# Performance work log

Hardware: AMD Instinct MI355X
Metric: run time of the kernel (lower is better)

## Reference

```python
import jax, jax.numpy as jnp
import numpy as np

NUM_NODES, NUM_RELS = 100000, 32
VOCAB = NUM_NODES + NUM_RELS
EMB, HID, LAYERS, CW = 128, 768, 4, 3
NHEAD, HDIM = HID // 64, 64
B, S = 4, 1024
T = S - 4 * CW  # rows where the full banded submask fits
EPS = 1e-5


def setup_inputs() -> dict:
    key = jax.random.key(0)
    ks = jax.random.split(key, 24)
    f32 = jnp.float32
    d = {}
    d["seq"] = jax.random.randint(ks[0], (B, S), 0, VOCAB)
    d["neg_ids"] = jax.random.randint(ks[1], (T, B), 0, VOCAB)
    # embedding + LayerNorm
    d["emb_table"] = jax.random.normal(ks[2], (VOCAB, EMB), f32)
    d["emb_ln_g"] = jnp.ones((EMB,), f32)
    d["emb_ln_b"] = jnp.zeros((EMB,), f32)
    # proj: Linear(EMB->HID) + GELU
    d["proj_w"] = jax.random.normal(ks[3], (HID, EMB), f32) * 0.02
    d["proj_b"] = jnp.zeros((HID,), f32)
    # transformer encoder layers (torch post-norm layout)
    d["wqkv"] = jax.random.normal(ks[4], (LAYERS, 3 * HID, HID), f32) * 0.02
    d["bqkv"] = jnp.zeros((LAYERS, 3 * HID), f32)
    d["wo"] = jax.random.normal(ks[5], (LAYERS, HID, HID), f32) * 0.02
    d["bo"] = jnp.zeros((LAYERS, HID), f32)
    d["ln1_g"] = jnp.ones((LAYERS, HID), f32)
    d["ln1_b"] = jnp.zeros((LAYERS, HID), f32)
    d["w1"] = jax.random.normal(ks[6], (LAYERS, 4 * HID, HID), f32) * 0.02
    d["b1"] = jnp.zeros((LAYERS, 4 * HID), f32)
    d["w2"] = jax.random.normal(ks[7], (LAYERS, HID, 4 * HID), f32) * 0.02
    d["b2"] = jnp.zeros((LAYERS, HID), f32)
    d["ln2_g"] = jnp.ones((LAYERS, HID), f32)
    d["ln2_b"] = jnp.zeros((LAYERS, HID), f32)
    # out: Linear(HID->EMB) + LayerNorm
    d["out_w"] = jax.random.normal(ks[8], (EMB, HID), f32) * 0.02
    d["out_b"] = jnp.zeros((EMB,), f32)
    d["out_ln_g"] = jnp.ones((EMB,), f32)
    d["out_ln_b"] = jnp.zeros((EMB,), f32)
    return d


def _ln(x, g, b):
    m = x.mean(-1, keepdims=True)
    v = x.var(-1, keepdims=True)
    return (x - m) * jax.lax.rsqrt(v + EPS) * g + b


def _pos_encoding(s, h):
    pos = jnp.arange(s, dtype=jnp.float32)[:, None]
    div = jnp.exp(jnp.arange(0, h, 2, dtype=jnp.float32) * (-jnp.log(10000.0) / h))
    ang = pos * div  # (S, H/2)
    pe = jnp.zeros((s, h), jnp.float32)
    pe = pe.at[:, 0::2].set(jnp.sin(ang)).at[:, 1::2].set(jnp.cos(ang))
    return pe[:, None, :]  # (S,1,H)


def _band_mask(s):
    i = jnp.arange(s)[:, None]
    j = jnp.arange(s)[None, :]
    gap = j - i
    allowed = (gap >= 0) & (gap <= 4 * CW) & (gap != 2 * CW)
    return jnp.where(allowed, 0.0, -jnp.inf).astype(jnp.float32)


def reference(seq, neg_ids, emb_table, emb_ln_g, emb_ln_b, proj_w, proj_b,
              wqkv, bqkv, wo, bo, ln1_g, ln1_b, w1, b1, w2, b2, ln2_g, ln2_b,
              out_w, out_b, out_ln_g, out_ln_b):
    seq_t = seq.T  # (S,B)
    s, b = seq_t.shape
    z = _ln(emb_table[seq_t], emb_ln_g, emb_ln_b)                 # (S,B,EMB)
    tokens = jax.nn.gelu(jnp.einsum('sbe,he->sbh', z, proj_w) + proj_b,
                         approximate=False)                        # (S,B,HID)
    tokens = tokens + _pos_encoding(s, HID)
    mask = _band_mask(s)                                           # (S,S)
    scale = 1.0 / jnp.sqrt(jnp.float32(HDIM))
    x = tokens
    for l in range(LAYERS):
        qkv = jnp.einsum('sbh,gh->sbg', x, wqkv[l]) + bqkv[l]      # (S,B,3H)
        q, k, v = [t.reshape(s, b, NHEAD, HDIM)
                   for t in jnp.split(qkv, 3, axis=-1)]
        scores = jnp.einsum('sbhd,tbhd->bhst', q, k) * scale + mask
        a = jax.nn.softmax(scores, axis=-1)                        # (B,H,S,S)
        attn = jnp.einsum('bhst,tbhd->sbhd', a, v).reshape(s, b, HID)
        attn = jnp.einsum('sbh,gh->sbg', attn, wo[l]) + bo[l]
        x = _ln(x + attn, ln1_g[l], ln1_b[l])
        ff = jax.nn.gelu(jnp.einsum('sbh,fh->sbf', x, w1[l]) + b1[l],
                         approximate=False)
        ff = jnp.einsum('sbf,hf->sbh', ff, w2[l]) + b2[l]
        x = _ln(x + ff, ln2_g[l], ln2_b[l])
    z_out = _ln(jnp.einsum('sbh,eh->sbe', x, out_w) + out_b,
                out_ln_g, out_ln_b)                                # (S,B,EMB)
    targets = jnp.arange(T) + CW + 1                               # (T,)
    z_hat = z_out[targets]                                         # (T,B,EMB)
    z_pos = z[targets]
    pos = jnp.sum(z_pos * z_hat, axis=-1).reshape(-1)              # (T*B,)
    z_neg = _ln(emb_table[neg_ids], emb_ln_g, emb_ln_b)            # (T,B,EMB)
    neg = jnp.sum(z_neg * z_hat, axis=-1).reshape(-1)              # (T*B,)
    # BCEWithLogitsLoss: labels 1 for pos, 0 for neg
    loss = (jnp.sum(jax.nn.softplus(-pos)) + jnp.sum(jax.nn.softplus(neg))) \
           / (pos.size + neg.size)
    return loss
```

## Files before the change

### kernel.cpp

```cpp
#include <hip/hip_runtime.h>
#include <hip/hip_bf16.h>
#include <math.h>

#define S_LEN 1024
#define B_DIM 4
#define EMB 128
#define HID 768
#define LAYERS 4
#define CW 3
#define NHEAD 12
#define HDIM 64
#define T_LEN (S_LEN - 4*CW)
#define LN_EPS 1e-5f
#define MROWS (S_LEN*B_DIM)

typedef unsigned short u16;
typedef __attribute__((ext_vector_type(8))) __bf16 bf16x8;
typedef __attribute__((ext_vector_type(4))) float f32x4;

__device__ __forceinline__ u16 f2b(float f){
    unsigned u = __float_as_uint(f);
    u += 0x7fff + ((u >> 16) & 1);
    return (u16)(u >> 16);
}
__device__ __forceinline__ float b2f(u16 h){
    return __uint_as_float(((unsigned)h) << 16);
}
__device__ __forceinline__ float gelu_exact(float x){
    return 0.5f * x * (1.0f + erff(x * 0.70710678118654752f));
}
__device__ __forceinline__ float softplus_f(float x){
    return fmaxf(x, 0.0f) + log1pf(expf(-fabsf(x)));
}
template<int N> __device__ __forceinline__ void waitcnt_vm(){
    if constexpr(N==0) asm volatile("s_waitcnt vmcnt(0)" ::: "memory");
    else if constexpr(N==2) asm volatile("s_waitcnt vmcnt(2)" ::: "memory");
    else if constexpr(N==3) asm volatile("s_waitcnt vmcnt(3)" ::: "memory");
    else if constexpr(N==4) asm volatile("s_waitcnt vmcnt(4)" ::: "memory");
    else if constexpr(N==6) asm volatile("s_waitcnt vmcnt(6)" ::: "memory");
    else if constexpr(N==8) asm volatile("s_waitcnt vmcnt(8)" ::: "memory");
}

__global__ void k_cvt(const float* __restrict__ w, u16* __restrict__ o, int n4){
    int i = blockIdx.x*256 + threadIdx.x;
    if(i >= n4) return;
    float4 v = *(const float4*)(w + (size_t)i*4);
    ushort4 t; t.x=f2b(v.x); t.y=f2b(v.y); t.z=f2b(v.z); t.w=f2b(v.w);
    *(ushort4*)(o + (size_t)i*4) = t;
}

__global__ void k_pe(float* __restrict__ pe){
    int idx = blockIdx.x*256 + threadIdx.x;
    if(idx >= S_LEN*HID) return;
    int s = idx / HID, c = idx % HID;
    int i2 = (c >> 1) * 2;
    float freq = expf(-(float)i2 * (logf(10000.0f) / (float)HID));
    float ang = (float)s * freq;
    pe[idx] = (c & 1) ? cosf(ang) : sinf(ang);
}

__global__ void k_embed_ln(const int* __restrict__ seq,
                           const float* __restrict__ emb,
                           const float* __restrict__ g,
                           const float* __restrict__ bta,
                           float* __restrict__ z, u16* __restrict__ zb){
    int row = blockIdx.x;
    int s = row >> 2, b = row & 3;
    int tok = seq[b*S_LEN + s];
    const float* e = emb + (size_t)tok * EMB;
    int lane = threadIdx.x;
    float v0 = e[lane], v1 = e[lane+64];
    float sum = v0+v1, sq = v0*v0+v1*v1;
    #pragma unroll
    for(int off=32; off; off>>=1){ sum += __shfl_xor(sum,off); sq += __shfl_xor(sq,off); }
    float m = sum * (1.0f/128.0f);
    float var = sq*(1.0f/128.0f) - m*m;
    float r = rsqrtf(var + LN_EPS);
    size_t base = (size_t)row*EMB;
    float o0 = (v0-m)*r*g[lane]    + bta[lane];
    float o1 = (v1-m)*r*g[lane+64] + bta[lane+64];
    z[base+lane] = o0; z[base+lane+64] = o1;
    zb[base+lane] = f2b(o0); zb[base+lane+64] = f2b(o1);
}

template<int BM, int BN, int THR, int SK, int EPI, int WF, int WB>
__global__ __launch_bounds__(THR) void k_mm(
    const u16*  __restrict__ A,
    const u16*  __restrict__ Bw,
    const float* __restrict__ bias,
    float* __restrict__ Cf, u16* __restrict__ Cb,
    int M, int N, int K, const float* __restrict__ pe)
{
    constexpr int WCOL = (THR==512) ? 4 : 2;
    constexpr int WM = BM/2, WN = BN/WCOL, MR = WM/16, NR = WN/16;
    constexpr int RA = (BM*4)/THR;
    constexpr int RB = (BN*4)/THR;
    constexpr int IC = RA + RB;
    static_assert(RA >= 1 && RB >= 1, "tile too small for THR");
    __shared__ u16 Al[3][BM*32];
    __shared__ u16 Bl[3][BN*32];
    int tid = threadIdx.x;
    int wave = tid >> 6, lane = tid & 63;

    int nbx = N / BN, nby = M / BM, nwg = nbx * nby * SK;
    int bid = blockIdx.x;
    int q = nwg >> 3, rm = nwg & 7, xcd = bid & 7, off = bid >> 3;
    int sbid = (xcd < rm ? xcd*(q+1) : rm*(q+1) + (xcd-rm)*q) + off;
    int slice = sbid / (nbx*nby);
    int rb2 = sbid % (nbx*nby);
    int row0 = (rb2 / nbx) * BM, col0 = (rb2 % nbx) * BN;
    int kb = slice * (K / SK);

    int wr = wave / WCOL, wc = wave % WCOL;
    int lr = lane & 15, lk = lane >> 4;

    f32x4 acc[MR][NR];
    #pragma unroll
    for(int m=0;m<MR;m++)
        #pragma unroll
        for(int n=0;n<NR;n++) acc[m][n] = (f32x4){0.f,0.f,0.f,0.f};

    const char* Abase = (const char*)A;
    const char* Bbase = (const char*)Bw;

    auto stage = [&](int buf, int k0){
        #pragma unroll
        for(int i=0;i<RA;i++){
            int p = i*(THR*16) + tid*16;
            int rr = p >> 6, u = (p >> 4) & 3;
            int us = u ^ ((rr >> 1) & 3);
            const char* g = Abase + ((size_t)(row0+rr)*K + k0)*2 + us*16;
            void* l = (char*)&Al[buf][0] + i*(THR*16) + wave*1024;
            __builtin_amdgcn_global_load_lds(
                (const __attribute__((address_space(1))) void*)g,
                (__attribute__((address_space(3))) void*)l, 16, 0, 0);
        }
        #pragma unroll
        for(int i=0;i<RB;i++){
            int p = i*(THR*16) + tid*16;
            int rr = p >> 6, u = (p >> 4) & 3;
            int us = u ^ ((rr >> 1) & 3);
            const char* g = Bbase + ((size_t)(col0+rr)*K + k0)*2 + us*16;
            void* l = (char*)&Bl[buf][0] + i*(THR*16) + wave*1024;
            __builtin_amdgcn_global_load_lds(
                (const __attribute__((address_space(1))) void*)g,
                (__attribute__((address_space(3))) void*)l, 16, 0, 0);
        }
    };

    int nt = (K / SK) >> 5;
    stage(0, kb);
    if(nt > 1) stage(1, kb + 32);
    int cur = 0;
    for(int t=0; t<nt; ++t){
        int pre = (cur==0) ? 2 : cur-1;
        if(t+2 < nt) stage(pre, kb + ((t+2) << 5));
        if(t+2 < nt)      waitcnt_vm<2*IC>();
        else if(t+1 < nt) waitcnt_vm<IC>();
        else              waitcnt_vm<0>();
        __builtin_amdgcn_s_barrier();
        __builtin_amdgcn_sched_barrier(0);
        bf16x8 af[MR], bfr[NR];
        #pragma unroll
        for(int m=0;m<MR;m++){
            int ar = wr*WM + m*16 + lr;
            af[m] = *(const bf16x8*)((const char*)&Al[cur][0] + ar*64 + ((lk ^ ((ar>>1)&3))<<4));
        }
        #pragma unroll
        for(int n=0;n<NR;n++){
            int br = wc*WN + n*16 + lr;
            bfr[n] = *(const bf16x8*)((const char*)&Bl[cur][0] + br*64 + ((lk ^ ((br>>1)&3))<<4));
        }
        __builtin_amdgcn_s_setprio(1);
        #pragma unroll
        for(int m=0;m<MR;m++)
            #pragma unroll
            for(int n=0;n<NR;n++)
                acc[m][n] = __builtin_amdgcn_mfma_f32_16x16x32_bf16(af[m], bfr[n], acc[m][n], 0, 0, 0);
        __builtin_amdgcn_s_setprio(0);
        __builtin_amdgcn_s_barrier();
        cur = (cur==2) ? 0 : cur+1;
    }
    #pragma unroll
    for(int m=0;m<MR;m++){
        #pragma unroll
        for(int n=0;n<NR;n++){
            #pragma unroll
            for(int j=0;j<4;j++){
                int row = row0 + wr*WM + m*16 + lk*4 + j;
                int col = col0 + wc*WN + n*16 + lr;
                float v = acc[m][n][j];
                if constexpr(EPI==3){
                    Cb[(size_t)slice*M*N + (size_t)row*N + col] = f2b(v);
                } else {
                    v += bias[col];
                    if(EPI==1) v = gelu_exact(v);
                    if(EPI==2) v = gelu_exact(v) + pe[(size_t)(row>>2)*HID + col];
                    if(WF) Cf[(size_t)row*N + col] = v;
                    if(WB) Cb[(size_t)row*N + col] = f2b(v);
                }
            }
        }
    }
}

__global__ __launch_bounds__(256) void k_attn(const u16* __restrict__ qkv,
                                              u16* __restrict__ out){
    __shared__ float P[4][16][36];
    int wv = threadIdx.x >> 6;
    int lane = threadIdx.x & 63;
    int wid = (blockIdx.x << 2) + wv;
    int h = wid % NHEAD;
    int b = (wid / NHEAD) & 3;
    int s0 = (wid / (NHEAD*B_DIM)) << 4;
    int lr = lane & 15, lk = lane >> 4;
    const int RS = 3*HID;

    bf16x8 qf[2], kf[2][2];
    #pragma unroll
    for(int kk=0;kk<2;kk++)
        qf[kk] = *(const bf16x8*)(qkv + (size_t)((s0+lr)*B_DIM + b)*RS + h*HDIM + kk*32 + lk*8);
    #pragma unroll
    for(int c=0;c<2;c++){
        int t = s0 + c*16 + lr; if(t > S_LEN-1) t = S_LEN-1;
        #pragma unroll
        for(int kk=0;kk<2;kk++)
            kf[c][kk] = *(const bf16x8*)(qkv + (size_t)(t*B_DIM + b)*RS + HID + h*HDIM + kk*32 + lk*8);
    }
    f32x4 acc0 = {0.f,0.f,0.f,0.f}, acc1 = {0.f,0.f,0.f,0.f};
    #pragma unroll
    for(int kk=0;kk<2;kk++){
        acc0 = __builtin_amdgcn_mfma_f32_16x16x32_bf16(qf[kk], kf[0][kk], acc0, 0,0,0);
        acc1 = __builtin_amdgcn_mfma_f32_16x16x32_bf16(qf[kk], kf[1][kk], acc1, 0,0,0);
    }
    float e0[4], e1[4], mx[4], sm[4];
    #pragma unroll
    for(int j=0;j<4;j++){
        int r = 4*lk + j;
        int g0 = lr - r, g1 = 16 + lr - r;
        bool a0 = (g0>=0) & (g0<=12) & (g0!=6);
        bool a1 = (g1>=0) & (g1<=12) & (g1!=6) & (s0+16+lr < S_LEN);
        e0[j] = a0 ? acc0[j]*0.125f : -INFINITY;
        e1[j] = a1 ? acc1[j]*0.125f : -INFINITY;
        mx[j] = fmaxf(e0[j], e1[j]);
    }
    #pragma unroll
    for(int off=1; off<16; off<<=1){
        #pragma unroll
        for(int j=0;j<4;j++) mx[j] = fmaxf(mx[j], __shfl_xor(mx[j], off));
    }
    #pragma unroll
    for(int j=0;j<4;j++){
        e0[j] = expf(e0[j]-mx[j]);
        e1[j] = expf(e1[j]-mx[j]);
        sm[j] = e0[j]+e1[j];
    }
    #pragma unroll
    for(int off=1; off<16; off<<=1){
        #pragma unroll
        for(int j=0;j<4;j++) sm[j] += __shfl_xor(sm[j], off);
    }
    #pragma unroll
    for(int j=0;j<4;j++){
        float inv = 1.0f/sm[j];
        int r = 4*lk + j;
        P[wv][r][lr]      = e0[j]*inv;
        P[wv][r][16+lr]   = e1[j]*inv;
    }
    float o[16];
    #pragma unroll
    for(int r=0;r<16;r++) o[r] = 0.f;
    #pragma unroll
    for(int g4=0; g4<32; g4+=4){
        float vr[4];
        #pragma unroll
        for(int qq=0;qq<4;qq++){
            int t = s0 + g4 + qq; if(t > S_LEN-1) t = S_LEN-1;
            vr[qq] = b2f(qkv[(size_t)(t*B_DIM + b)*RS + 2*HID + h*HDIM + lane]);
        }
        #pragma unroll
        for(int r=0;r<16;r++){
            f32x4 w = *(const f32x4*)&P[wv][r][g4];
            o[r] = fmaf(w[0], vr[0], fmaf(w[1], vr[1], fmaf(w[2], vr[2], fmaf(w[3], vr[3], o[r]))));
        }
    }
    #pragma unroll
    for(int r=0;r<16;r++)
        out[(size_t)((s0+r)*B_DIM + b)*HID + h*HDIM + lane] = f2b(o[r]);
}

__global__ __launch_bounds__(192) void k_add_ln768_2(
    u16* __restrict__ xb, const u16* __restrict__ y,
    const float* __restrict__ ybias,
    const float* __restrict__ g, const float* __restrict__ bta)
{
    const size_t SL = (size_t)MROWS*HID;
    int row = blockIdx.x;
    size_t base = (size_t)row * HID;
    int tid = threadIdx.x;
    int c = tid * 4;
    ushort4 xv = *(const ushort4*)(xb + base + c);
    ushort4 y0 = *(const ushort4*)(y + base + c);
    ushort4 y1 = *(const ushort4*)(y + SL + base + c);
    float4 bb = *(const float4*)(ybias + c);
    float v0 = b2f(xv.x)+b2f(y0.x)+b2f(y1.x)+bb.x;
    float v1 = b2f(xv.y)+b2f(y0.y)+b2f(y1.y)+bb.y;
    float v2 = b2f(xv.z)+b2f(y0.z)+b2f(y1.z)+bb.z;
    float v3 = b2f(xv.w)+b2f(y0.w)+b2f(y1.w)+bb.w;
    float sum = v0+v1+v2+v3;
    float sq  = v0*v0+v1*v1+v2*v2+v3*v3;
    #pragma unroll
    for(int off=32; off; off>>=1){ sum+=__shfl_xor(sum,off); sq+=__shfl_xor(sq,off); }
    __shared__ float s1[3], s2[3];
    int w = tid>>6;
    if((tid&63)==0){ s1[w]=sum; s2[w]=sq; }
    __syncthreads();
    sum = s1[0]+s1[1]+s1[2];
    sq  = s2[0]+s2[1]+s2[2];
    float m = sum*(1.f/768.f);
    float var = sq*(1.f/768.f) - m*m;
    float r = rsqrtf(var+LN_EPS);
    float4 gv = *(const float4*)(g + c);
    float4 bv = *(const float4*)(bta + c);
    ushort4 o;
    o.x = f2b((v0-m)*r*gv.x + bv.x);
    o.y = f2b((v1-m)*r*gv.y + bv.y);
    o.z = f2b((v2-m)*r*gv.z + bv.z);
    o.w = f2b((v3-m)*r*gv.w + bv.w);
    *(ushort4*)(xb + base + c) = o;
}

__global__ __launch_bounds__(256) void k_loss(
    const float* __restrict__ zout, const float* __restrict__ z,
    const int* __restrict__ neg_ids, const float* __restrict__ emb,
    const float* __restrict__ eg, const float* __restrict__ eb,
    const float* __restrict__ og, const float* __restrict__ ob,
    float* __restrict__ loss)
{
    int wv = threadIdx.x >> 6, lane = threadIdx.x & 63;
    int it0 = blockIdx.x*16 + wv*4;
    float h0r[4], h1r[4], z0[4], z1[4], ee0[4], ee1[4];
    #pragma unroll
    for(int i=0;i<4;i++){
        int it = it0 + i;
        int t = it >> 2, b = it & 3;
        int s = t + CW + 1;
        size_t hb = (size_t)(s*B_DIM+b)*EMB;
        h0r[i] = zout[hb+lane]; h1r[i] = zout[hb+lane+64];
        z0[i]  = z[hb+lane];    z1[i]  = z[hb+lane+64];
        int nid = neg_ids[it];
        const float* e = emb + (size_t)nid*EMB;
        ee0[i] = e[lane]; ee1[i] = e[lane+64];
    }
    float local = 0.f;
    #pragma unroll
    for(int i=0;i<4;i++){
        float hsum = h0r[i]+h1r[i], hsq = h0r[i]*h0r[i]+h1r[i]*h1r[i];
        float esum = ee0[i]+ee1[i], esq = ee0[i]*ee0[i]+ee1[i]*ee1[i];
        #pragma unroll
        for(int off=32; off; off>>=1){
            hsum += __shfl_xor(hsum,off);
            hsq  += __shfl_xor(hsq,off);
            esum += __shfl_xor(esum,off);
            esq  += __shfl_xor(esq,off);
        }
        float hm = hsum*(1.f/128.f), hvar = hsq*(1.f/128.f)-hm*hm, hr = rsqrtf(hvar+LN_EPS);
        float h0 = (h0r[i]-hm)*hr*og[lane]    + ob[lane];
        float h1 = (h1r[i]-hm)*hr*og[lane+64] + ob[lane+64];
        float em = esum*(1.f/128.f), evar = esq*(1.f/128.f)-em*em, er = rsqrtf(evar+LN_EPS);
        float zn0 = (ee0[i]-em)*er*eg[lane]    + eb[lane];
        float zn1 = (ee1[i]-em)*er*eg[lane+64] + eb[lane+64];
        float pv = z0[i]*h0 + z1[i]*h1;
        float nv = zn0*h0 + zn1*h1;
        #pragma unroll
        for(int off=32; off; off>>=1){
            pv += __shfl_xor(pv,off);
            nv += __shfl_xor(nv,off);
        }
        if(lane==0) local += softplus_f(-pv) + softplus_f(nv);
    }
    __shared__ float ls[4];
    if(lane==0) ls[wv] = local;
    __syncthreads();
    if(threadIdx.x==0){
        float v = ls[0]+ls[1]+ls[2]+ls[3];
        atomicAdd(loss, v * (1.0f/(2.0f*T_LEN*B_DIM)));
    }
}

static inline int cvt_grid(size_t n){ return (int)((n/4 + 255)/256); }

extern "C" void kernel_launch(void* const* d_in, const int* in_sizes, int n_in,
                              void* d_out, int out_size, void* d_ws, size_t ws_size,
                              hipStream_t stream) {
    const int*   seq      = (const int*)  d_in[0];
    const int*   neg_ids  = (const int*)  d_in[1];
    const float* emb      = (const float*)d_in[2];
    const float* emb_ln_g = (const float*)d_in[3];
    const float* emb_ln_b = (const float*)d_in[4];
    const float* proj_w   = (const float*)d_in[5];
    const float* proj_b   = (const float*)d_in[6];
    const float* wqkv     = (const float*)d_in[7];
    const float* bqkv     = (const float*)d_in[8];
    const float* wo       = (const float*)d_in[9];
    const float* bo       = (const float*)d_in[10];
    const float* ln1_g    = (const float*)d_in[11];
    const float* ln1_b    = (const float*)d_in[12];
    const float* w1       = (const float*)d_in[13];
    const float* b1       = (const float*)d_in[14];
    const float* w2       = (const float*)d_in[15];
    const float* b2       = (const float*)d_in[16];
    const float* ln2_g    = (const float*)d_in[17];
    const float* ln2_b    = (const float*)d_in[18];
    const float* out_w    = (const float*)d_in[19];
    const float* out_b    = (const float*)d_in[20];
    const float* out_ln_g = (const float*)d_in[21];
    const float* out_ln_b = (const float*)d_in[22];

    const size_t NPROJ = (size_t)HID*EMB;
    const size_t NQKV  = (size_t)3*HID*HID;
    const size_t NWO   = (size_t)HID*HID;
    const size_t NW1   = (size_t)4*HID*HID;
    const size_t NW2   = (size_t)4*HID*HID;
    const size_t NOUT  = (size_t)EMB*HID;

    char* p = (char*)d_ws;
    float* pe   = (float*)p; p += (size_t)S_LEN*HID*4;
    float* z    = (float*)p; p += (size_t)MROWS*EMB*4;
    float* zout = (float*)p; p += (size_t)MROWS*EMB*4;
    u16*  z_b   = (u16*)p;   p += (size_t)MROWS*EMB*2;
    u16*  x_b   = (u16*)p;   p += (size_t)MROWS*HID*2;
    u16*  at_b  = (u16*)p;   p += (size_t)MROWS*HID*2;
    u16*  y_b   = (u16*)p;   p += (size_t)2*MROWS*HID*2;
    u16*  big   = (u16*)p;   p += (size_t)MROWS*3072*2;
    size_t act_bytes = (size_t)(p - (char*)d_ws);

    size_t full_w_elems = NPROJ + NOUT + LAYERS*(NQKV + NWO + NW1 + NW2);
    bool full = ws_size >= act_bytes + full_w_elems*2;
    size_t fb_elems = NPROJ + NOUT + NQKV + NWO + NW1 + NW2;
    if(!full && ws_size < act_bytes + fb_elems*2) return;

    u16* wbase = (u16*)p;
    u16 *wp_proj, *wp_out, *wp_qkv0, *wp_wo0, *wp_w10, *wp_w20;
    size_t sq, so, s1o, s2o;
    if(full){
        u16* q0 = wbase;
        wp_proj = q0;                 q0 += NPROJ;
        wp_out  = q0;                 q0 += NOUT;
        wp_qkv0 = q0;                 q0 += LAYERS*NQKV;
        wp_wo0  = q0;                 q0 += LAYERS*NWO;
        wp_w10  = q0;                 q0 += LAYERS*NW1;
        wp_w20  = q0;                 q0 += LAYERS*NW2;
        sq = NQKV; so = NWO; s1o = NW1; s2o = NW2;
    } else {
        u16* q0 = wbase;
        wp_proj = q0;                 q0 += NPROJ;
        wp_out  = q0;                 q0 += NOUT;
        wp_qkv0 = q0;                 q0 += NQKV;
        wp_wo0  = q0;                 q0 += NWO;
        wp_w10  = q0;                 q0 += NW1;
        wp_w20  = q0;                 q0 += NW2;
        sq = so = s1o = s2o = 0;
    }

    hipMemsetAsync(d_out, 0, sizeof(float), stream);

    k_pe<<<(S_LEN*HID+255)/256, 256, 0, stream>>>(pe);
    k_embed_ln<<<MROWS, 64, 0, stream>>>(seq, emb, emb_ln_g, emb_ln_b, z, z_b);

    k_cvt<<<cvt_grid(NPROJ), 256, 0, stream>>>(proj_w, wp_proj, (int)(NPROJ/4));
    k_cvt<<<cvt_grid(NOUT),  256, 0, stream>>>(out_w,  wp_out,  (int)(NOUT/4));
    if(full){
        k_cvt<<<cvt_grid(LAYERS*NQKV), 256, 0, stream>>>(wqkv, wp_qkv0, (int)(LAYERS*NQKV/4));
        k_cvt<<<cvt_grid(LAYERS*NWO),  256, 0, stream>>>(wo,   wp_wo0,  (int)(LAYERS*NWO/4));
        k_cvt<<<cvt_grid(LAYERS*NW1),  256, 0, stream>>>(w1,   wp_w10,  (int)(LAYERS*NW1/4));
        k_cvt<<<cvt_grid(LAYERS*NW2),  256, 0, stream>>>(w2,   wp_w20,  (int)(LAYERS*NW2/4));
    }

    k_mm<128,64,256,1,2,0,1><<<(768/64)*(MROWS/128), 256, 0, stream>>>(
        z_b, wp_proj, proj_b, nullptr, x_b, MROWS, HID, EMB, pe);

    for(int l=0; l<LAYERS; ++l){
        if(!full){
            k_cvt<<<cvt_grid(NQKV), 256, 0, stream>>>(wqkv + (size_t)l*NQKV, wp_qkv0, (int)(NQKV/4));
            k_cvt<<<cvt_grid(NWO),  256, 0, stream>>>(wo   + (size_t)l*NWO,  wp_wo0,  (int)(NWO/4));
            k_cvt<<<cvt_grid(NW1),  256, 0, stream>>>(w1   + (size_t)l*NW1,  wp_w10,  (int)(NW1/4));
            k_cvt<<<cvt_grid(NW2),  256, 0, stream>>>(w2   + (size_t)l*NW2,  wp_w20,  (int)(NW2/4));
        }
        k_mm<128,128,512,1,0,0,1><<<(2304/128)*(MROWS/128), 512, 0, stream>>>(
            x_b, wp_qkv0 + (size_t)l*sq, bqkv + l*2304, nullptr, big, MROWS, 2304, HID, nullptr);
        k_attn<<<(S_LEN/16)*B_DIM*NHEAD/4, 256, 0, stream>>>(big, at_b);
        k_mm<128,64,256,2,3,0,0><<<(768/64)*(MROWS/128)*2, 256, 0, stream>>>(
            at_b, wp_wo0 + (size_t)l*so, nullptr, nullptr, y_b, MROWS, HID, HID, nullptr);
        k_add_ln768_2<<<MROWS, 192, 0, stream>>>(x_b, y_b, bo + l*HID,
                                                 ln1_g + l*HID, ln1_b + l*HID);
        k_mm<128,128,512,1,1,0,1><<<(3072/128)*(MROWS/128), 512, 0, stream>>>(
            x_b, wp_w10 + (size_t)l*s1o, b1 + l*3072, nullptr, big, MROWS, 3072, HID, nullptr);
        k_mm<128,64,256,2,3,0,0><<<(768/64)*(MROWS/128)*2, 256, 0, stream>>>(
            big, wp_w20 + (size_t)l*s2o, nullptr, nullptr, y_b, MROWS, HID, 3072, nullptr);
        k_add_ln768_2<<<MROWS, 192, 0, stream>>>(x_b, y_b, b2 + l*HID,
                                                 ln2_g + l*HID, ln2_b + l*HID);
    }
    k_mm<64,64,256,1,0,1,0><<<(EMB/64)*(MROWS/64), 256, 0, stream>>>(
        x_b, wp_out, out_b, zout, nullptr, MROWS, EMB, HID, nullptr);
    k_loss<<<(T_LEN*B_DIM)/16, 256, 0, stream>>>(zout, z, neg_ids, emb,
                                                 emb_ln_g, emb_ln_b, out_ln_g, out_ln_b,
                                                 (float*)d_out);
}
```

Before: 591.3 us.

## Add BK=64 double-buffered GEMM path for 256-thread matmuls

Makes the GEMM K-tile size a template parameter. With BK=64 the kernel stages 128-byte rows with an XOR swizzle over 8 chunks, uses double buffering instead of triple, and runs two MFMA sub-steps per barrier pair. The 256-thread GEMMs (proj, Wo, W2, out) move to BK=64, halving barrier and wait count per K. The trade is a shallower prefetch pipeline and more LDS per buffer, which may hurt latency hiding or occupancy.

After: 546.3 us. 7.6% less time.

```diff
diff --git a/kernel.cpp b/kernel.cpp
--- a/kernel.cpp
+++ b/kernel.cpp
@@ -39,6 +39,7 @@
     else if constexpr(N==4) asm volatile("s_waitcnt vmcnt(4)" ::: "memory");
     else if constexpr(N==6) asm volatile("s_waitcnt vmcnt(6)" ::: "memory");
     else if constexpr(N==8) asm volatile("s_waitcnt vmcnt(8)" ::: "memory");
+    else if constexpr(N==12) asm volatile("s_waitcnt vmcnt(12)" ::: "memory");
 }
 
 __global__ void k_cvt(const float* __restrict__ w, u16* __restrict__ o, int n4){
@@ -83,7 +84,7 @@
     zb[base+lane] = f2b(o0); zb[base+lane+64] = f2b(o1);
 }
 
-template<int BM, int BN, int THR, int SK, int EPI, int WF, int WB>
+template<int BM, int BN, int BK, int THR, int SK, int EPI, int WF, int WB>
 __global__ __launch_bounds__(THR) void k_mm(
     const u16*  __restrict__ A,
     const u16*  __restrict__ Bw,
@@ -93,12 +94,15 @@
 {
     constexpr int WCOL = (THR==512) ? 4 : 2;
     constexpr int WM = BM/2, WN = BN/WCOL, MR = WM/16, NR = WN/16;
-    constexpr int RA = (BM*4)/THR;
-    constexpr int RB = (BN*4)/THR;
+    constexpr int ROWB = BK*2;
+    constexpr int CM = ROWB/16 - 1;
+    constexpr int RA = (BM*ROWB)/(THR*16);
+    constexpr int RB = (BN*ROWB)/(THR*16);
     constexpr int IC = RA + RB;
+    constexpr int NBUF = (BK==32) ? 3 : 2;
     static_assert(RA >= 1 && RB >= 1, "tile too small for THR");
-    __shared__ u16 Al[3][BM*32];
-    __shared__ u16 Bl[3][BN*32];
+    __shared__ u16 Al[NBUF][BM*BK];
+    __shared__ u16 Bl[NBUF][BN*BK];
     int tid = threadIdx.x;
     int wave = tid >> 6, lane = tid & 63;
 
@@ -123,12 +127,16 @@
     const char* Abase = (const char*)A;
     const char* Bbase = (const char*)Bw;
 
+    auto swz = [](int u, int rr)->int{
+        if constexpr(BK==32) return u ^ ((rr>>1)&3);
+        else                 return u ^ (rr & CM);
+    };
     auto stage = [&](int buf, int k0){
         #pragma unroll
         for(int i=0;i<RA;i++){
             int p = i*(THR*16) + tid*16;
-            int rr = p >> 6, u = (p >> 4) & 3;
-            int us = u ^ ((rr >> 1) & 3);
+            int rr = p / ROWB, u = (p >> 4) & CM;
+            int us = swz(u, rr);
             const char* g = Abase + ((size_t)(row0+rr)*K + k0)*2 + us*16;
             void* l = (char*)&Al[buf][0] + i*(THR*16) + wave*1024;
             __builtin_amdgcn_global_load_lds(
@@ -138,8 +146,8 @@
         #pragma unroll
         for(int i=0;i<RB;i++){
             int p = i*(THR*16) + tid*16;
-            int rr = p >> 6, u = (p >> 4) & 3;
-            int us = u ^ ((rr >> 1) & 3);
+            int rr = p / ROWB, u = (p >> 4) & CM;
+            int us = swz(u, rr);
             const char* g = Bbase + ((size_t)(col0+rr)*K + k0)*2 + us*16;
             void* l = (char*)&Bl[buf][0] + i*(THR*16) + wave*1024;
             __builtin_amdgcn_global_load_lds(
@@ -148,38 +156,49 @@
         }
     };
 
-    int nt = (K / SK) >> 5;
+    int nt = (K / SK) / BK;
     stage(0, kb);
-    if(nt > 1) stage(1, kb + 32);
+    if(NBUF==3 && nt > 1) stage(1, kb + BK);
     int cur = 0;
     for(int t=0; t<nt; ++t){
-        int pre = (cur==0) ? 2 : cur-1;
-        if(t+2 < nt) stage(pre, kb + ((t+2) << 5));
-        if(t+2 < nt)      waitcnt_vm<2*IC>();
-        else if(t+1 < nt) waitcnt_vm<IC>();
-        else              waitcnt_vm<0>();
+        if constexpr(NBUF==3){
+            int pre = (cur==0) ? 2 : cur-1;
+            if(t+2 < nt) stage(pre, kb + (t+2)*BK);
+            if(t+2 < nt)      waitcnt_vm<2*IC>();
+            else if(t+1 < nt) waitcnt_vm<IC>();
+            else              waitcnt_vm<0>();
+        } else {
+            if(t+1 < nt){ stage(cur^1, kb + (t+1)*BK); waitcnt_vm<IC>(); }
+            else        { waitcnt_vm<0>(); }
+        }
         __builtin_amdgcn_s_barrier();
         __builtin_amdgcn_sched_barrier(0);
-        bf16x8 af[MR], bfr[NR];
-        #pragma unroll
-        for(int m=0;m<MR;m++){
-            int ar = wr*WM + m*16 + lr;
-            af[m] = *(const bf16x8*)((const char*)&Al[cur][0] + ar*64 + ((lk ^ ((ar>>1)&3))<<4));
-        }
-        #pragma unroll
-        for(int n=0;n<NR;n++){
-            int br = wc*WN + n*16 + lr;
-            bfr[n] = *(const bf16x8*)((const char*)&Bl[cur][0] + br*64 + ((lk ^ ((br>>1)&3))<<4));
-        }
-        __builtin_amdgcn_s_setprio(1);
-        #pragma unroll
-        for(int m=0;m<MR;m++)
+        #pragma unroll
+        for(int kk=0; kk<BK/32; ++kk){
+            bf16x8 af[MR], bfr[NR];
             #pragma unroll
-            for(int n=0;n<NR;n++)
-                acc[m][n] = __builtin_amdgcn_mfma_f32_16x16x32_bf16(af[m], bfr[n], acc[m][n], 0, 0, 0);
-        __builtin_amdgcn_s_setprio(0);
+            for(int m=0;m<MR;m++){
+                int ar = wr*WM + m*16 + lr;
+                int c  = swz(kk*4 + lk, ar);
+                af[m] = *(const bf16x8*)((const char*)&Al[cur][0] + ar*ROWB + (c<<4));
+            }
+            #pragma unroll
+            for(int n=0;n<NR;n++){
+                int br = wc*WN + n*16 + lr;
+                int c  = swz(kk*4 + lk, br);
+                bfr[n] = *(const bf16x8*)((const char*)&Bl[cur][0] + br*ROWB + (c<<4));
+            }
+            __builtin_amdgcn_s_setprio(1);
+            #pragma unroll
+            for(int m=0;m<MR;m++)
+                #pragma unroll
+                for(int n=0;n<NR;n++)
+                    acc[m][n] = __builtin_amdgcn_mfma_f32_16x16x32_bf16(af[m], bfr[n], acc[m][n], 0, 0, 0);
+            __builtin_amdgcn_s_setprio(0);
+        }
         __builtin_amdgcn_s_barrier();
-        cur = (cur==2) ? 0 : cur+1;
+        if constexpr(NBUF==3) cur = (cur==2) ? 0 : cur+1;
+        else                  cur ^= 1;
     }
     #pragma unroll
     for(int m=0;m<MR;m++){
@@ -477,7 +496,7 @@
         k_cvt<<<cvt_grid(LAYERS*NW2),  256, 0, stream>>>(w2,   wp_w20,  (int)(LAYERS*NW2/4));
     }
 
-    k_mm<128,64,256,1,2,0,1><<<(768/64)*(MROWS/128), 256, 0, stream>>>(
+    k_mm<128,64,64,256,1,2,0,1><<<(768/64)*(MROWS/128), 256, 0, stream>>>(
         z_b, wp_proj, proj_b, nullptr, x_b, MROWS, HID, EMB, pe);
 
     for(int l=0; l<LAYERS; ++l){
@@ -487,21 +506,21 @@
             k_cvt<<<cvt_grid(NW1),  256, 0, stream>>>(w1   + (size_t)l*NW1,  wp_w10,  (int)(NW1/4));
             k_cvt<<<cvt_grid(NW2),  256, 0, stream>>>(w2   + (size_t)l*NW2,  wp_w20,  (int)(NW2/4));
         }
-        k_mm<128,128,512,1,0,0,1><<<(2304/128)*(MROWS/128), 512, 0, stream>>>(
+        k_mm<128,128,32,512,1,0,0,1><<<(2304/128)*(MROWS/128), 512, 0, stream>>>(
             x_b, wp_qkv0 + (size_t)l*sq, bqkv + l*2304, nullptr, big, MROWS, 2304, HID, nullptr);
         k_attn<<<(S_LEN/16)*B_DIM*NHEAD/4, 256, 0, stream>>>(big, at_b);
-        k_mm<128,64,256,2,3,0,0><<<(768/64)*(MROWS/128)*2, 256, 0, stream>>>(
+        k_mm<128,64,64,256,2,3,0,0><<<(768/64)*(MROWS/128)*2, 256, 0, stream>>>(
             at_b, wp_wo0 + (size_t)l*so, nullptr, nullptr, y_b, MROWS, HID, HID, nullptr);
         k_add_ln768_2<<<MROWS, 192, 0, stream>>>(x_b, y_b, bo + l*HID,
                                                  ln1_g + l*HID, ln1_b + l*HID);
-        k_mm<128,128,512,1,1,0,1><<<(3072/128)*(MROWS/128), 512, 0, stream>>>(
+        k_mm<128,128,32,512,1,1,0,1><<<(3072/128)*(MROWS/128), 512, 0, stream>>>(
             x_b, wp_w10 + (size_t)l*s1o, b1 + l*3072, nullptr, big, MROWS, 3072, HID, nullptr);
-        k_mm<128,64,256,2,3,0,0><<<(768/64)*(MROWS/128)*2, 256, 0, stream>>>(
+        k_mm<128,64,64,256,2,3,0,0><<<(768/64)*(MROWS/128)*2, 256, 0, stream>>>(
             big, wp_w20 + (size_t)l*s2o, nullptr, nullptr, y_b, MROWS, HID, 3072, nullptr);
         k_add_ln768_2<<<MROWS, 192, 0, stream>>>(x_b, y_b, b2 + l*HID,
                                                  ln2_g + l*HID, ln2_b + l*HID);
     }
-    k_mm<64,64,256,1,0,1,0><<<(EMB/64)*(MROWS/64), 256, 0, stream>>>(
+    k_mm<64,64,64,256,1,0,1,0><<<(EMB/64)*(MROWS/64), 256, 0, stream>>>(
         x_b, wp_out, out_b, zout, nullptr, MROWS, EMB, HID, nullptr);
     k_loss<<<(T_LEN*B_DIM)/16, 256, 0, stream>>>(zout, z, neg_ids, emb,
                                                  emb_ln_g, emb_ln_b, out_ln_g, out_ln_b,
```
